# Kernel optimization log

Hardware: AMD Instinct MI355X
Metric: run time of the kernel (lower is better)

The kernel has to match this reference:

```python
import jax, jax.numpy as jnp
import numpy as np

N_EMBD = 1024
N_HEAD = 16
HEAD = N_EMBD // N_HEAD
B, T = 4, 2048


def setup_inputs() -> dict:
    key = jax.random.key(0)
    k1, k2, k3, k4, k5 = jax.random.split(key, 5)
    s = 1.0 / np.sqrt(N_EMBD)
    x = jax.random.normal(k1, (B, T, N_EMBD), dtype=jnp.float32)
    W_qkv = jax.random.uniform(k2, (N_EMBD, 3 * N_EMBD), jnp.float32, -s, s)
    b_qkv = jax.random.uniform(k3, (3 * N_EMBD,), jnp.float32, -s, s)
    W_out = jax.random.uniform(k4, (N_EMBD, N_EMBD), jnp.float32, -s, s)
    b_out = jax.random.uniform(k5, (N_EMBD,), jnp.float32, -s, s)
    return {"x": x, "W_qkv": W_qkv, "b_qkv": b_qkv, "W_out": W_out, "b_out": b_out}


def reference(x, W_qkv, b_qkv, W_out, b_out):
    Bx, Tx, C = x.shape
    qkv = x @ W_qkv + b_qkv                      # [B,T,3C]
    q, k, v = jnp.split(qkv, 3, axis=-1)
    def to_heads(t):
        return t.reshape(Bx, Tx, N_HEAD, HEAD).transpose(0, 2, 1, 3)  # [B,H,T,hd]
    q, k, v = to_heads(q), to_heads(k), to_heads(v)
    scores = jnp.einsum('bhqd,bhkd->bhqk', q, k) / np.sqrt(HEAD)
    causal = jnp.tril(jnp.ones((Tx, Tx), dtype=bool))
    scores = jnp.where(causal[None, None, :, :], scores, jnp.float32(-1e9))
    attn = jax.nn.softmax(scores, axis=-1)       # dropout p=0 (eval)
    out = jnp.einsum('bhqk,bhkd->bhqd', attn, v)
    out = out.transpose(0, 2, 1, 3).reshape(Bx, Tx, C)
    return out @ W_out + b_out
```

## Files before the change

kernel.cpp:

```cpp
#include <hip/hip_runtime.h>

typedef __attribute__((ext_vector_type(8))) short short8;
typedef __attribute__((ext_vector_type(8))) _Float16 half8;
typedef __attribute__((ext_vector_type(4))) float f32x4;
typedef __attribute__((ext_vector_type(16))) float f32x16;
typedef __attribute__((ext_vector_type(4))) unsigned uint4v;
typedef __attribute__((ext_vector_type(2))) float float2v;

#define MFMA_BF16(a, b, c) __builtin_amdgcn_mfma_f32_16x16x32_bf16(a, b, c, 0, 0, 0)
#define MFMA32_BF16(a, b, c) __builtin_amdgcn_mfma_f32_32x32x16_bf16(a, b, c, 0, 0, 0)
#define MFMA32_F16(a, b, c) __builtin_amdgcn_mfma_f32_32x32x16_f16(a, b, c, 0, 0, 0)

#define GLD16(g, l)                                                          \
  __builtin_amdgcn_global_load_lds(                                          \
      (const __attribute__((address_space(1))) unsigned int*)(g),            \
      (__attribute__((address_space(3))) unsigned int*)(l), 16, 0, 0)

__device__ __forceinline__ unsigned short f2bf(float f) {
  unsigned int u = __float_as_uint(f);
  u += 0x7fffu + ((u >> 16) & 1u);
  return (unsigned short)(u >> 16);
}

__global__ __launch_bounds__(256) void prep_k(const float* __restrict__ x,
                                              unsigned short* __restrict__ xb,
                                              const float* __restrict__ W_qkv,
                                              unsigned short* __restrict__ wqkvT,
                                              const float* __restrict__ W_out,
                                              unsigned short* __restrict__ woutT) {
  __shared__ float tile[64][65];
  const int blk = blockIdx.x;
  const int tid = threadIdx.x;
  if (blk < 8192) {
    int i = blk * 256 + tid;
    float4 v = reinterpret_cast<const float4*>(x)[i];
    ushort4 o;
    o.x = f2bf(v.x); o.y = f2bf(v.y); o.z = f2bf(v.z); o.w = f2bf(v.w);
    reinterpret_cast<ushort4*>(xb)[i] = o;
    return;
  }
  const float* W;
  unsigned short* Wt;
  int N, bx;
  if (blk < 8960) { W = W_qkv; Wt = wqkvT; N = 3072; bx = blk - 8192; }
  else            { W = W_out; Wt = woutT; N = 1024; bx = blk - 8960; }
  const int tk = (bx & 15) * 64;
  const int tn = (bx >> 4) * 64;
#pragma unroll
  for (int c = 0; c < 4; ++c) {
    int k = c * 16 + (tid >> 4);
    int n = (tid & 15) * 4;
    float4 v = *reinterpret_cast<const float4*>(&W[(size_t)(tk + k) * N + tn + n]);
    tile[k][n] = v.x; tile[k][n + 1] = v.y; tile[k][n + 2] = v.z; tile[k][n + 3] = v.w;
  }
  __syncthreads();
#pragma unroll
  for (int p = 0; p < 2; ++p) {
    int n = p * 32 + (tid >> 3);
    int k = (tid & 7) * 8;
    ushort4 a, b;
    a.x = f2bf(tile[k + 0][n]); a.y = f2bf(tile[k + 1][n]);
    a.z = f2bf(tile[k + 2][n]); a.w = f2bf(tile[k + 3][n]);
    b.x = f2bf(tile[k + 4][n]); b.y = f2bf(tile[k + 5][n]);
    b.z = f2bf(tile[k + 6][n]); b.w = f2bf(tile[k + 7][n]);
    *reinterpret_cast<ushort4*>(&Wt[(size_t)(tn + n) * 1024 + tk + k]) = a;
    *reinterpret_cast<ushort4*>(&Wt[(size_t)(tn + n) * 1024 + tk + k + 4]) = b;
  }
}

template <int MODE>
__global__ __launch_bounds__(512, 2) void gemm8(const unsigned short* __restrict__ A,
                                                const unsigned short* __restrict__ Bt,
                                                const float* __restrict__ bias,
                                                float* __restrict__ outF,
                                                unsigned short* __restrict__ q_ws,
                                                unsigned short* __restrict__ k_ws,
                                                unsigned short* __restrict__ vt_ws,
                                                int N) {
  constexpr int K = 1024;
  __shared__ unsigned short As[3][256 * 64];
  __shared__ unsigned short Bs[3][128 * 64];
  const int tid = threadIdx.x;
  const int wave = tid >> 6, lane = tid & 63;
  const int quad = lane >> 4, l15 = lane & 15;
  const int m0 = blockIdx.x * 256, n0 = blockIdx.y * 128;
  const int wm = (wave & 3) * 64, wn = (wave >> 2) * 64;

  const f32x4 zf = {0.f, 0.f, 0.f, 0.f};
  f32x4 acc[4][4];
#pragma unroll
  for (int i = 0; i < 4; ++i)
#pragma unroll
    for (int j = 0; j < 4; ++j) acc[i][j] = zf;

  const int rr = tid >> 3;
  const int scol = ((tid & 7) ^ (rr & 7)) * 8;
  const int swz = l15 & 7;
  const unsigned short* Arow = &A[(size_t)(m0 + rr) * K + scol];
  const unsigned short* Brow = &Bt[(size_t)(n0 + rr) * K + scol];

#pragma unroll
  for (int tt = 0; tt < 2; ++tt) {
#pragma unroll
    for (int c = 0; c < 4; ++c)
      GLD16(Arow + (size_t)c * 64 * K + tt * 64, &As[tt][c * 4096 + tid * 8]);
#pragma unroll
    for (int c = 0; c < 2; ++c)
      GLD16(Brow + (size_t)c * 64 * K + tt * 64, &Bs[tt][c * 4096 + tid * 8]);
  }

  for (int t = 0; t < 16; ++t) {
    const int cur = t % 3, fut = (t + 2) % 3;
    const int pf = (t + 2 < 16) ? t + 2 : 15;
#pragma unroll
    for (int c = 0; c < 4; ++c)
      GLD16(Arow + (size_t)c * 64 * K + pf * 64, &As[fut][c * 4096 + tid * 8]);
#pragma unroll
    for (int c = 0; c < 2; ++c)
      GLD16(Brow + (size_t)c * 64 * K + pf * 64, &Bs[fut][c * 4096 + tid * 8]);
    asm volatile("s_waitcnt vmcnt(12)\n\ts_barrier" ::: "memory");

#pragma unroll
    for (int kk = 0; kk < 2; ++kk) {
      const int ch = (kk * 4 + quad) ^ swz;
      short8 af[4], bg[4];
#pragma unroll
      for (int i = 0; i < 4; ++i)
        af[i] = *reinterpret_cast<const short8*>(&As[cur][(wm + i * 16 + l15) * 64 + ch * 8]);
#pragma unroll
      for (int j = 0; j < 4; ++j)
        bg[j] = *reinterpret_cast<const short8*>(&Bs[cur][(wn + j * 16 + l15) * 64 + ch * 8]);
      __builtin_amdgcn_s_setprio(1);
#pragma unroll
      for (int i = 0; i < 4; ++i)
#pragma unroll
        for (int j = 0; j < 4; ++j) acc[i][j] = MFMA_BF16(af[i], bg[j], acc[i][j]);
      __builtin_amdgcn_s_setprio(0);
    }
    asm volatile("s_barrier" ::: "memory");
  }
  asm volatile("s_waitcnt vmcnt(0)" ::: "memory");

  const float kScQ = 0.125f * 1.44269504088896f;
  const int cls = n0 >> 10;
#pragma unroll
  for (int i = 0; i < 4; ++i) {
#pragma unroll
    for (int j = 0; j < 4; ++j) {
      const int n = n0 + wn + j * 16 + l15;
      const float bv = bias[n];
      const int mb = m0 + wm + i * 16 + quad * 4;
      if (MODE == 1) {
#pragma unroll
        for (int r = 0; r < 4; ++r) outF[(size_t)(mb + r) * N + n] = acc[i][j][r] + bv;
      } else if (cls == 0) {
        const int b = mb >> 11, t0 = mb & 2047;
        const int h = n >> 6, d = n & 63;
#pragma unroll
        for (int r = 0; r < 4; ++r)
          q_ws[(((size_t)(b * 16 + h)) * 2048 + t0 + r) * 64 + d] =
              f2bf((acc[i][j][r] + bv) * kScQ);
      } else if (cls == 1) {
        const int b = mb >> 11, t0 = mb & 2047;
        const int n2 = n - 1024, h = n2 >> 6, d = n2 & 63;
#pragma unroll
        for (int r = 0; r < 4; ++r)
          k_ws[(((size_t)(b * 16 + h)) * 2048 + t0 + r) * 64 + d] = f2bf(acc[i][j][r] + bv);
      } else {
        const int b = mb >> 11, t0 = mb & 2047;
        const int n2 = n - 2048, h = n2 >> 6, d = n2 & 63;
        uint2 pk;
        pk.x = __builtin_bit_cast(unsigned int,
                                  __builtin_amdgcn_cvt_pkrtz(acc[i][j][0] + bv, acc[i][j][1] + bv));
        pk.y = __builtin_bit_cast(unsigned int,
                                  __builtin_amdgcn_cvt_pkrtz(acc[i][j][2] + bv, acc[i][j][3] + bv));
        *reinterpret_cast<uint2*>(
            &vt_ws[(((size_t)(b * 16 + h)) * 64 + d) * 2048 + t0]) = pk;
      }
    }
  }
}

__global__ __launch_bounds__(256, 3) void attn_k(const unsigned short* __restrict__ q_ws,
                                                 const unsigned short* __restrict__ k_ws,
                                                 const unsigned short* __restrict__ vt_ws,
                                                 unsigned short* __restrict__ att_ws) {
  const int T = 2048;
  const int bid = blockIdx.x;
  const int bh = (bid & 7) * 8 + ((bid >> 3) & 7);
  const int s = 15 - (bid >> 6);
  const int tid = threadIdx.x;
  const int wv = tid >> 6, lane = tid & 63;
  const int L = lane & 31, hl = lane >> 5;

  const unsigned short* Qh = q_ws + (size_t)bh * T * 64;
  const unsigned short* Kh = k_ws + (size_t)bh * T * 64;
  const _Float16* Vh = (const _Float16*)vt_ws + (size_t)bh * 64 * T;
  const int b = bh >> 4, h = bh & 15;

  __shared__ unsigned short Ks[2][64 * 64];
  __shared__ _Float16 Vs[2][64 * 64];

  const int qw = s * 4 + wv;
  const int q0 = qw * 32;
  const int diagTile = qw >> 1;
  const int nk = 2 * s + 2;
  const int myq = q0 + L;

  short8 qb[4];
#pragma unroll
  for (int kk = 0; kk < 4; ++kk)
    qb[kk] = *reinterpret_cast<const short8*>(&Qh[(size_t)(q0 + L) * 64 + kk * 16 + hl * 8]);

  f32x16 o0 = {}, o1 = {};
  float2v li = {0.f, 0.f};

  const int srow8 = tid >> 3;
  const int schunk = (tid & 7) ^ (srow8 & 7);

  GLD16(&Kh[(size_t)srow8 * 64 + schunk * 8], &Ks[0][tid * 8]);
  GLD16(&Kh[(size_t)(32 + srow8) * 64 + schunk * 8], &Ks[0][2048 + tid * 8]);
  GLD16(&Vh[(size_t)srow8 * T + schunk * 8], &Vs[0][tid * 8]);
  GLD16(&Vh[(size_t)(32 + srow8) * T + schunk * 8], &Vs[0][2048 + tid * 8]);

  auto softmax32 = [&](const f32x16& scc, unsigned (&pwc)[4][2]) {
#pragma unroll
    for (int g = 0; g < 4; ++g) {
      float2v e01, e23;
      e01[0] = __builtin_amdgcn_exp2f(scc[4 * g + 0]);
      e01[1] = __builtin_amdgcn_exp2f(scc[4 * g + 1]);
      e23[0] = __builtin_amdgcn_exp2f(scc[4 * g + 2]);
      e23[1] = __builtin_amdgcn_exp2f(scc[4 * g + 3]);
      float2v s2;
      asm("v_pk_add_f32 %0, %1, %2" : "=v"(s2) : "v"(e01), "v"(e23));
      asm("v_pk_add_f32 %0, %0, %1" : "+v"(li) : "v"(s2));
      pwc[g][0] = __builtin_bit_cast(unsigned int, __builtin_amdgcn_cvt_pkrtz(e01[0], e01[1]));
      pwc[g][1] = __builtin_bit_cast(unsigned int, __builtin_amdgcn_cvt_pkrtz(e23[0], e23[1]));
    }
#pragma unroll
    for (int r = 0; r < 2; ++r) {
      asm volatile("v_permlane32_swap_b32 %0, %1" : "+v"(pwc[0][r]), "+v"(pwc[1][r]));
      asm volatile("v_permlane32_swap_b32 %0, %1" : "+v"(pwc[2][r]), "+v"(pwc[3][r]));
    }
  };

  for (int kt = 0; kt < nk; ++kt) {
    const int cur = kt & 1, nxt = cur ^ 1;
    if (kt) asm volatile("s_barrier" ::: "memory");
    const int pf = (kt + 1 < nk) ? kt + 1 : nk - 1;
    GLD16(&Kh[(size_t)(pf * 64 + srow8) * 64 + schunk * 8], &Ks[nxt][tid * 8]);
    GLD16(&Kh[(size_t)(pf * 64 + 32 + srow8) * 64 + schunk * 8], &Ks[nxt][2048 + tid * 8]);
    GLD16(&Vh[(size_t)srow8 * T + pf * 64 + schunk * 8], &Vs[nxt][tid * 8]);
    GLD16(&Vh[(size_t)(32 + srow8) * T + pf * 64 + schunk * 8], &Vs[nxt][2048 + tid * 8]);
    asm volatile("s_waitcnt vmcnt(4)\n\ts_barrier" ::: "memory");

    if (kt <= diagTile) {
      const unsigned short* KsC = Ks[cur];
      const _Float16* VsC = Vs[cur];
      const int kb = kt * 64;

      f32x16 sc0 = {}, sc1 = {};
      __builtin_amdgcn_s_setprio(1);
#pragma unroll
      for (int kk = 0; kk < 4; ++kk) {
        const int sl = ((kk * 2 + hl) ^ (L & 7)) * 8;
        short8 k0 = *reinterpret_cast<const short8*>(&KsC[L * 64 + sl]);
        short8 k1 = *reinterpret_cast<const short8*>(&KsC[(32 + L) * 64 + sl]);
        sc0 = MFMA32_BF16(k0, qb[kk], sc0);
        sc1 = MFMA32_BF16(k1, qb[kk], sc1);
      }
      __builtin_amdgcn_s_setprio(0);

      half8 vr0[2], vr1[2];
#pragma unroll
      for (int t = 0; t < 2; ++t) {
        const int sl = ((t * 2 + hl) ^ (L & 7)) * 8;
        vr0[t] = *reinterpret_cast<const half8*>(&VsC[L * 64 + sl]);
        vr1[t] = *reinterpret_cast<const half8*>(&VsC[(32 + L) * 64 + sl]);
      }

      if (kt == diagTile) {
#pragma unroll
        for (int reg = 0; reg < 16; ++reg) {
          const int row = (reg & 3) + 8 * (reg >> 2) + 4 * hl;
          sc0[reg] = (kb + row > myq) ? -1e30f : sc0[reg];
        }
      }
      unsigned pw0[4][2], pw1[4][2];
      softmax32(sc0, pw0);

      half8 vr2[2], vr3[2];
#pragma unroll
      for (int t = 2; t < 4; ++t) {
        const int sl = ((t * 2 + hl) ^ (L & 7)) * 8;
        vr2[t - 2] = *reinterpret_cast<const half8*>(&VsC[L * 64 + sl]);
        vr3[t - 2] = *reinterpret_cast<const half8*>(&VsC[(32 + L) * 64 + sl]);
      }

      __builtin_amdgcn_s_setprio(1);
      {
        uint4v f0 = {pw0[0][0], pw0[0][1], pw0[1][0], pw0[1][1]};
        uint4v f1 = {pw0[2][0], pw0[2][1], pw0[3][0], pw0[3][1]};
        half8 pb0 = __builtin_bit_cast(half8, f0);
        half8 pb1 = __builtin_bit_cast(half8, f1);
        o0 = MFMA32_F16(vr0[0], pb0, o0);
        o1 = MFMA32_F16(vr1[0], pb0, o1);
        o0 = MFMA32_F16(vr0[1], pb1, o0);
        o1 = MFMA32_F16(vr1[1], pb1, o1);
      }
      __builtin_amdgcn_s_setprio(0);

      if (kt == diagTile) {
#pragma unroll
        for (int reg = 0; reg < 16; ++reg) {
          const int row = (reg & 3) + 8 * (reg >> 2) + 4 * hl;
          sc1[reg] = (kb + 32 + row > myq) ? -1e30f : sc1[reg];
        }
      }
      softmax32(sc1, pw1);

      __builtin_amdgcn_s_setprio(1);
      {
        uint4v f0 = {pw1[0][0], pw1[0][1], pw1[1][0], pw1[1][1]};
        uint4v f1 = {pw1[2][0], pw1[2][1], pw1[3][0], pw1[3][1]};
        half8 pb0 = __builtin_bit_cast(half8, f0);
        half8 pb1 = __builtin_bit_cast(half8, f1);
        o0 = MFMA32_F16(vr2[0], pb0, o0);
        o1 = MFMA32_F16(vr3[0], pb0, o1);
        o0 = MFMA32_F16(vr2[1], pb1, o0);
        o1 = MFMA32_F16(vr3[1], pb1, o1);
      }
      __builtin_amdgcn_s_setprio(0);
    }
  }
  asm volatile("s_waitcnt vmcnt(0)" ::: "memory");

  float l_i = li[0] + li[1];
  l_i += __shfl_xor(l_i, 32);
  const float inv = 1.f / l_i;
#pragma unroll
  for (int sg = 0; sg < 2; ++sg) {
    const f32x16& oo = sg ? o1 : o0;
#pragma unroll
    for (int g = 0; g < 4; ++g) {
      const int d0 = sg * 32 + g * 8 + hl * 4;
      uint2 ov;
      ov.x = (unsigned)f2bf(oo[4 * g + 0] * inv) | ((unsigned)f2bf(oo[4 * g + 1] * inv) << 16);
      ov.y = (unsigned)f2bf(oo[4 * g + 2] * inv) | ((unsigned)f2bf(oo[4 * g + 3] * inv) << 16);
      *reinterpret_cast<uint2*>(
          &att_ws[(size_t)(b * 2048 + q0 + L) * 1024 + h * 64 + d0]) = ov;
    }
  }
}

extern "C" void kernel_launch(void* const* d_in, const int* in_sizes, int n_in,
                              void* d_out, int out_size, void* d_ws, size_t ws_size,
                              hipStream_t stream) {
  (void)in_sizes; (void)n_in; (void)out_size; (void)ws_size;
  const float* x     = (const float*)d_in[0];
  const float* W_qkv = (const float*)d_in[1];
  const float* b_qkv = (const float*)d_in[2];
  const float* W_out = (const float*)d_in[3];
  const float* b_out = (const float*)d_in[4];
  float* out = (float*)d_out;

  char* ws = (char*)d_ws;
  unsigned short* xb    = (unsigned short*)(ws);
  unsigned short* wqkvT = (unsigned short*)(ws + 16777216);
  unsigned short* woutT = (unsigned short*)(ws + 23068672);
  unsigned short* q_ws  = (unsigned short*)(ws + 25165824);
  unsigned short* k_ws  = (unsigned short*)(ws + 41943040);
  unsigned short* vt_ws = (unsigned short*)(ws + 58720256);
  unsigned short* attb  = (unsigned short*)(ws + 75497472);

  prep_k<<<9216, 256, 0, stream>>>(x, xb, W_qkv, wqkvT, W_out, woutT);

  dim3 g1(32, 24);
  gemm8<0><<<g1, 512, 0, stream>>>(xb, wqkvT, b_qkv, nullptr, q_ws, k_ws, vt_ws, 3072);

  attn_k<<<1024, 256, 0, stream>>>(q_ws, k_ws, vt_ws, attb);

  dim3 g2(32, 8);
  gemm8<1><<<g2, 512, 0, stream>>>(attb, woutT, b_out, out, nullptr, nullptr, nullptr, 1024);
}
```

Baseline: 245.2 us.

## Replace QKV projection GEMM with simpler 128x128-tile single-buffered kernel

Adds a new templated bf16 MFMA GEMM (gemm_bt) that uses 128xBN tiles, 256 threads, swizzled LDS layout and direct global-to-LDS loads, and uses it for the QKV projection in place of the 256x128 triple-buffered 512-thread gemm8. The epilogue scatters Q (pre-scaled), K and transposed V into their head-major workspaces as before. The goal is more blocks and better occupancy and load balance for this shape. In exchange it gives up the multi-stage prefetch pipelining, which may expose load latency.

```diff
diff --git a/kernel.cpp b/kernel.cpp
--- a/kernel.cpp
+++ b/kernel.cpp
@@ -65,6 +65,104 @@
     b.z = f2bf(tile[k + 6][n]); b.w = f2bf(tile[k + 7][n]);
     *reinterpret_cast<ushort4*>(&Wt[(size_t)(tn + n) * 1024 + tk + k]) = a;
     *reinterpret_cast<ushort4*>(&Wt[(size_t)(tn + n) * 1024 + tk + k + 4]) = b;
+  }
+}
+
+template <int MODE, int BN>
+__global__ __launch_bounds__(256) void gemm_bt(const unsigned short* __restrict__ A,
+                                               const unsigned short* __restrict__ Bt,
+                                               const float* __restrict__ bias,
+                                               float* __restrict__ outF,
+                                               unsigned short* __restrict__ q_ws,
+                                               unsigned short* __restrict__ k_ws,
+                                               unsigned short* __restrict__ vt_ws,
+                                               int M, int N, int K) {
+  constexpr int NJ = BN / 32;
+  constexpr int NBC = BN * 64 / 2048;
+  __shared__ unsigned short As[128 * 64];
+  __shared__ unsigned short Bs[BN * 64];
+
+  const int tid = threadIdx.x;
+  const int wave = tid >> 6, lane = tid & 63;
+  const int quad = lane >> 4, l15 = lane & 15;
+  const int m0 = blockIdx.x * 128, n0 = blockIdx.y * BN;
+  const int wm = (wave & 1) * 64, wn = (wave >> 1) * (BN / 2);
+
+  const f32x4 zf = {0.f, 0.f, 0.f, 0.f};
+  f32x4 acc[4][NJ];
+#pragma unroll
+  for (int i = 0; i < 4; ++i)
+#pragma unroll
+    for (int j = 0; j < NJ; ++j) acc[i][j] = zf;
+
+  const int rr = tid >> 3;
+  const int scol = ((tid & 7) ^ (rr & 7)) * 8;
+  const int swz = l15 & 7;
+
+  for (int kt = 0; kt < K; kt += 64) {
+    __syncthreads();
+#pragma unroll
+    for (int c = 0; c < 4; ++c)
+      GLD16(&A[(size_t)(m0 + c * 32 + rr) * K + kt + scol], &As[c * 2048 + tid * 8]);
+#pragma unroll
+    for (int c = 0; c < NBC; ++c)
+      GLD16(&Bt[(size_t)(n0 + c * 32 + rr) * K + kt + scol], &Bs[c * 2048 + tid * 8]);
+    __syncthreads();
+
+#pragma unroll
+    for (int kk = 0; kk < 2; ++kk) {
+      const int ch = (kk * 4 + quad) ^ swz;
+      short8 af[4], bg[NJ];
+#pragma unroll
+      for (int i = 0; i < 4; ++i)
+        af[i] = *reinterpret_cast<const short8*>(&As[(wm + i * 16 + l15) * 64 + ch * 8]);
+#pragma unroll
+      for (int j = 0; j < NJ; ++j)
+        bg[j] = *reinterpret_cast<const short8*>(&Bs[(wn + j * 16 + l15) * 64 + ch * 8]);
+#pragma unroll
+      for (int i = 0; i < 4; ++i)
+#pragma unroll
+        for (int j = 0; j < NJ; ++j) acc[i][j] = MFMA_BF16(af[i], bg[j], acc[i][j]);
+    }
+  }
+
+  const float kScQ = 0.125f * 1.44269504088896f;
+  const int cls = n0 >> 10;
+#pragma unroll
+  for (int i = 0; i < 4; ++i) {
+#pragma unroll
+    for (int j = 0; j < NJ; ++j) {
+      const int n = n0 + wn + j * 16 + l15;
+      const float bv = bias[n];
+      const int mb = m0 + wm + i * 16 + quad * 4;
+      if (MODE == 1) {
+#pragma unroll
+        for (int r = 0; r < 4; ++r) outF[(size_t)(mb + r) * N + n] = acc[i][j][r] + bv;
+      } else if (cls == 0) {
+        const int b = mb >> 11, t0 = mb & 2047;
+        const int h = n >> 6, d = n & 63;
+#pragma unroll
+        for (int r = 0; r < 4; ++r)
+          q_ws[(((size_t)(b * 16 + h)) * 2048 + t0 + r) * 64 + d] =
+              f2bf((acc[i][j][r] + bv) * kScQ);
+      } else if (cls == 1) {
+        const int b = mb >> 11, t0 = mb & 2047;
+        const int n2 = n - 1024, h = n2 >> 6, d = n2 & 63;
+#pragma unroll
+        for (int r = 0; r < 4; ++r)
+          k_ws[(((size_t)(b * 16 + h)) * 2048 + t0 + r) * 64 + d] = f2bf(acc[i][j][r] + bv);
+      } else {
+        const int b = mb >> 11, t0 = mb & 2047;
+        const int n2 = n - 2048, h = n2 >> 6, d = n2 & 63;
+        uint2 pk;
+        pk.x = __builtin_bit_cast(unsigned int,
+                                  __builtin_amdgcn_cvt_pkrtz(acc[i][j][0] + bv, acc[i][j][1] + bv));
+        pk.y = __builtin_bit_cast(unsigned int,
+                                  __builtin_amdgcn_cvt_pkrtz(acc[i][j][2] + bv, acc[i][j][3] + bv));
+        *reinterpret_cast<uint2*>(
+            &vt_ws[(((size_t)(b * 16 + h)) * 64 + d) * 2048 + t0]) = pk;
+      }
+    }
   }
 }
 
@@ -375,8 +473,9 @@
 
   prep_k<<<9216, 256, 0, stream>>>(x, xb, W_qkv, wqkvT, W_out, woutT);
 
-  dim3 g1(32, 24);
-  gemm8<0><<<g1, 512, 0, stream>>>(xb, wqkvT, b_qkv, nullptr, q_ws, k_ws, vt_ws, 3072);
+  dim3 g1(64, 24);
+  gemm_bt<0, 128><<<g1, 256, 0, stream>>>(xb, wqkvT, b_qkv, nullptr, q_ws, k_ws, vt_ws,
+                                          8192, 3072, 1024);
 
   attn_k<<<1024, 256, 0, stream>>>(q_ws, k_ws, vt_ws, attb);
 
```

Result: faster. 234.4 us, median of 2 (-4.4%).
